# Optimization experiments

Measured on AMD Instinct MI355X. Metric: run time of the kernel, lower is better.

The kernel has to match this reference:

```python
import jax, jax.numpy as jnp
import numpy as np

N = 50000
E = 1600000
D_IN = 256
D_OUT = 256
NUM_SAMPLES = 5
LN_EPS = 1e-5


def setup_inputs() -> dict:
    key = jax.random.key(0)
    ks = jax.random.split(key, 6)
    x = jax.random.normal(ks[0], (N, D_IN), dtype=jnp.float32)
    adj_indices = jax.random.randint(ks[1], (2, E), 0, N, dtype=jnp.int32)
    adj_values = jax.random.uniform(ks[2], (E,), dtype=jnp.float32)
    mask = jax.random.uniform(ks[3], (NUM_SAMPLES, D_OUT), dtype=jnp.float32)
    # Xavier-uniform init as in reset_parameters
    limit_w = float(np.sqrt(6.0 / (D_IN + D_OUT)))
    weight = jax.random.uniform(ks[4], (D_IN, D_OUT), dtype=jnp.float32,
                                minval=-limit_w, maxval=limit_w)
    limit_b = float(np.sqrt(6.0 / (1 + D_OUT)))
    bias = jax.random.uniform(ks[5], (1, D_OUT), dtype=jnp.float32,
                              minval=-limit_b, maxval=limit_b)
    ln_gamma = jnp.ones((D_OUT,), dtype=jnp.float32)
    ln_beta = jnp.zeros((D_OUT,), dtype=jnp.float32)
    return {"x": x, "adj_indices": adj_indices, "adj_values": adj_values,
            "mask": mask, "weight": weight, "bias": bias,
            "ln_gamma": ln_gamma, "ln_beta": ln_beta}


def reference(x, adj_indices, adj_values, mask, weight, bias, ln_gamma, ln_beta):
    # dense transform: [N, D_in] @ [D_in, D_out]
    h = x @ weight
    # sparse adjacency spmm (COO): out[r] += v_e * h[c] for each edge e=(r,c)
    rows, cols = adj_indices[0], adj_indices[1]
    h = jax.ops.segment_sum(adj_values[:, None] * h[cols], rows, num_segments=N)
    # bias + ELU
    h = jax.nn.elu(h + bias)
    # LayerNorm over feature dim
    mu = jnp.mean(h, axis=-1, keepdims=True)
    var = jnp.var(h, axis=-1, keepdims=True)
    h = (h - mu) * jax.lax.rsqrt(var + LN_EPS) * ln_gamma + ln_beta
    # expand to num_samples and apply per-sample mask: [N, S, D_out]
    out = h[:, None, :] * mask[None, :, :]
    return out
```

## Files before the change

kernel.cpp:

```cpp
#include <hip/hip_runtime.h>
#include <math.h>

#define NNODES 50000
#define D 256
#define NSAMP 5
#define LN_EPS 1e-5f
#define NB 196
#define BCAP 9216
#define ACHUNK 8192

typedef __bf16 bf16;
typedef __attribute__((ext_vector_type(8))) __bf16 bf16x8;
typedef __attribute__((ext_vector_type(4))) float f32x4;
typedef unsigned long long u64;

__device__ inline float bflo(unsigned int u) { return __uint_as_float(u << 16); }
__device__ inline float bfhi(unsigned int u) { return __uint_as_float(u & 0xffff0000u); }

__device__ inline u64 packrec(int r, int c, float v) {
    return (u64)(unsigned int)(c | (r << 16)) | ((u64)__float_as_uint(v) << 32);
}

__global__ void prep_kernel(const float* __restrict__ w, bf16* __restrict__ wt,
                            int* __restrict__ bcur) {
    const int b = blockIdx.x;
    if (b < D) {
        const int k = threadIdx.x;
        wt[(size_t)b * D + k] = (bf16)w[(size_t)k * D + b];
    } else {
        if (threadIdx.x < NB) bcur[threadIdx.x] = 0;
    }
}

__global__ __launch_bounds__(256) void gemm_binA_kernel(const float* __restrict__ x,
                                                        const bf16* __restrict__ wt,
                                                        bf16* __restrict__ h,
                                                        const int* __restrict__ rows,
                                                        const int* __restrict__ cols,
                                                        const float* __restrict__ vals,
                                                        int* __restrict__ bcur,
                                                        u64* __restrict__ binned,
                                                        int AB, int E) {
    if ((int)blockIdx.x < AB) {
        __shared__ int hist[NB];
        __shared__ int base[NB];
        for (int i = threadIdx.x; i < NB; i += 256) hist[i] = 0;
        __syncthreads();
        const int e0 = blockIdx.x * ACHUNK;
        const int e1 = min(e0 + ACHUNK, E);
        for (int e = e0 + threadIdx.x; e < e1; e += 256)
            atomicAdd(&hist[rows[e] >> 8], 1);
        __syncthreads();
        for (int i = threadIdx.x; i < NB; i += 256) {
            const int c = hist[i];
            base[i] = c ? atomicAdd(&bcur[i], c) : 0;
            hist[i] = 0;
        }
        __syncthreads();
        for (int e = e0 + threadIdx.x; e < e1; e += 256) {
            const int r = rows[e];
            const int b = r >> 8;
            const int k = base[b] + atomicAdd(&hist[b], 1);
            if (k < BCAP)
                binned[(size_t)b * BCAP + k] = packrec(r, cols[e], vals[e]);
        }
        return;
    }

    const int gb = blockIdx.x - AB;
    const int wave = threadIdx.x >> 6;
    const int lane = threadIdx.x & 63;
    const int row0 = gb * 64 + wave * 16;
    const int am = lane & 15;
    const int ag = lane >> 4;

    int arow = row0 + am;
    if (arow >= NNODES) arow = NNODES - 1;

    f32x4 acc[16];
#pragma unroll
    for (int n = 0; n < 16; ++n) acc[n] = (f32x4){0.f, 0.f, 0.f, 0.f};

#pragma unroll
    for (int kk = 0; kk < 8; ++kk) {
        const int kb = kk * 32 + ag * 8;
        const float* xp = x + (size_t)arow * D + kb;
        const f32x4 a0 = __builtin_nontemporal_load((const f32x4*)xp);
        const f32x4 a1 = __builtin_nontemporal_load((const f32x4*)(xp + 4));
        bf16x8 a;
        a[0] = (bf16)a0[0]; a[1] = (bf16)a0[1]; a[2] = (bf16)a0[2]; a[3] = (bf16)a0[3];
        a[4] = (bf16)a1[0]; a[5] = (bf16)a1[1]; a[6] = (bf16)a1[2]; a[7] = (bf16)a1[3];
#pragma unroll
        for (int n = 0; n < 16; ++n) {
            const bf16x8 b = *(const bf16x8*)(wt + (size_t)(n * 16 + am) * D + kb);
            acc[n] = __builtin_amdgcn_mfma_f32_16x16x32_bf16(a, b, acc[n], 0, 0, 0);
        }
    }

    const int drow = row0 + ag * 4;
#pragma unroll
    for (int r = 0; r < 4; ++r) {
        if (drow + r < NNODES) {
            bf16* hp = h + (size_t)(drow + r) * D + am;
#pragma unroll
            for (int n = 0; n < 16; ++n) hp[n * 16] = (bf16)acc[n][r];
        }
    }
}

__global__ __launch_bounds__(256) void sortB_kernel(const u64* __restrict__ binned,
                                                    const int* __restrict__ bcur,
                                                    u64* __restrict__ sorted,
                                                    int* __restrict__ rstart,
                                                    int* __restrict__ rcnt) {
    const int b = blockIdx.x;
    const int tid = threadIdx.x;
    const int cnt_b = min(bcur[b], BCAP);
    const u64* src = binned + (size_t)b * BCAP;

    __shared__ int hist[256];
    __shared__ int s[256];
    hist[tid] = 0;
    __syncthreads();
    for (int i = tid; i < cnt_b; i += 256)
        atomicAdd(&hist[(int)((src[i] >> 16) & 255)], 1);
    __syncthreads();
    const int v = hist[tid];
    s[tid] = v;
    __syncthreads();
    for (int d = 1; d < 256; d <<= 1) {
        const int t = (tid >= d) ? s[tid - d] : 0;
        __syncthreads();
        s[tid] += t;
        __syncthreads();
    }
    const int excl = s[tid] - v;
    const int r = b * 256 + tid;
    if (r < NNODES) {
        rstart[r] = b * BCAP + excl;
        rcnt[r]   = v;
    }
    hist[tid] = excl;
    __syncthreads();
    for (int i = tid; i < cnt_b; i += 256) {
        const u64 rec = src[i];
        const int k = atomicAdd(&hist[(int)((rec >> 16) & 255)], 1);
        sorted[(size_t)b * BCAP + k] = rec;
    }
}

__global__ __launch_bounds__(256) void row_kernel(const unsigned short* __restrict__ hb,
                                                  const int* __restrict__ rstart,
                                                  const int* __restrict__ rcnt,
                                                  const u64* __restrict__ ep,
                                                  const float* __restrict__ bias,
                                                  const float* __restrict__ gamma,
                                                  const float* __restrict__ beta,
                                                  const float* __restrict__ mask,
                                                  float* __restrict__ out, int n) {
    const int wave = threadIdx.x >> 6;
    const int lane = threadIdx.x & 63;
    const int r = blockIdx.x * 4 + wave;
    if (r >= n) return;

    const int s = rstart[r];
    const int e = s + rcnt[r];

    float a0 = 0.f, a1 = 0.f, a2 = 0.f, a3 = 0.f;
    int i = s;
    for (; i + 3 < e; i += 4) {
        const u64 e0 = ep[i], e1 = ep[i + 1], e2 = ep[i + 2], e3 = ep[i + 3];
        const int c0 = (int)(e0 & 0xFFFF), c1 = (int)(e1 & 0xFFFF);
        const int c2 = (int)(e2 & 0xFFFF), c3 = (int)(e3 & 0xFFFF);
        const uint2 q0 = *(const uint2*)(hb + (size_t)c0 * D + lane * 4);
        const uint2 q1 = *(const uint2*)(hb + (size_t)c1 * D + lane * 4);
        const uint2 q2 = *(const uint2*)(hb + (size_t)c2 * D + lane * 4);
        const uint2 q3 = *(const uint2*)(hb + (size_t)c3 * D + lane * 4);
        const float v0 = __uint_as_float((unsigned int)(e0 >> 32));
        const float v1 = __uint_as_float((unsigned int)(e1 >> 32));
        const float v2 = __uint_as_float((unsigned int)(e2 >> 32));
        const float v3 = __uint_as_float((unsigned int)(e3 >> 32));
        a0 += v0 * bflo(q0.x) + v1 * bflo(q1.x) + v2 * bflo(q2.x) + v3 * bflo(q3.x);
        a1 += v0 * bfhi(q0.x) + v1 * bfhi(q1.x) + v2 * bfhi(q2.x) + v3 * bfhi(q3.x);
        a2 += v0 * bflo(q0.y) + v1 * bflo(q1.y) + v2 * bflo(q2.y) + v3 * bflo(q3.y);
        a3 += v0 * bfhi(q0.y) + v1 * bfhi(q1.y) + v2 * bfhi(q2.y) + v3 * bfhi(q3.y);
    }
    for (; i < e; ++i) {
        const u64 e0 = ep[i];
        const int c0 = (int)(e0 & 0xFFFF);
        const uint2 q0 = *(const uint2*)(hb + (size_t)c0 * D + lane * 4);
        const float v0 = __uint_as_float((unsigned int)(e0 >> 32));
        a0 += v0 * bflo(q0.x);
        a1 += v0 * bfhi(q0.x);
        a2 += v0 * bflo(q0.y);
        a3 += v0 * bfhi(q0.y);
    }

    const f32x4 b4 = *(const f32x4*)(bias + lane * 4);
    float x0 = a0 + b4[0], x1 = a1 + b4[1], x2 = a2 + b4[2], x3 = a3 + b4[3];
    x0 = x0 > 0.f ? x0 : expm1f(x0);
    x1 = x1 > 0.f ? x1 : expm1f(x1);
    x2 = x2 > 0.f ? x2 : expm1f(x2);
    x3 = x3 > 0.f ? x3 : expm1f(x3);

    float s1 = x0 + x1 + x2 + x3;
    float s2 = x0 * x0 + x1 * x1 + x2 * x2 + x3 * x3;
#pragma unroll
    for (int d = 1; d < 64; d <<= 1) {
        s1 += __shfl_xor(s1, d);
        s2 += __shfl_xor(s2, d);
    }
    const float mu   = s1 * (1.f / 256.f);
    const float var  = s2 * (1.f / 256.f) - mu * mu;
    const float rsig = rsqrtf(var + LN_EPS);

    const f32x4 g4  = *(const f32x4*)(gamma + lane * 4);
    const f32x4 be4 = *(const f32x4*)(beta + lane * 4);
    const float y0 = (x0 - mu) * rsig * g4[0] + be4[0];
    const float y1 = (x1 - mu) * rsig * g4[1] + be4[1];
    const float y2 = (x2 - mu) * rsig * g4[2] + be4[2];
    const float y3 = (x3 - mu) * rsig * g4[3] + be4[3];

#pragma unroll
    for (int smp = 0; smp < NSAMP; ++smp) {
        const f32x4 m4 = *(const f32x4*)(mask + smp * D + lane * 4);
        f32x4 o;
        o[0] = y0 * m4[0];
        o[1] = y1 * m4[1];
        o[2] = y2 * m4[2];
        o[3] = y3 * m4[3];
        __builtin_nontemporal_store(o, (f32x4*)(out + ((size_t)r * NSAMP + smp) * D + lane * 4));
    }
}

extern "C" void kernel_launch(void* const* d_in, const int* in_sizes, int n_in,
                              void* d_out, int out_size, void* d_ws, size_t ws_size,
                              hipStream_t stream) {
    const float* x     = (const float*)d_in[0];
    const int*   adj   = (const int*)d_in[1];
    const float* vals  = (const float*)d_in[2];
    const float* mask  = (const float*)d_in[3];
    const float* w     = (const float*)d_in[4];
    const float* bias  = (const float*)d_in[5];
    const float* gamma = (const float*)d_in[6];
    const float* beta  = (const float*)d_in[7];
    float*       out   = (float*)d_out;

    const int N = NNODES;
    const int E = in_sizes[2];
    const int GB = (N + 63) / 64;
    const int AB = (E + ACHUNK - 1) / ACHUNK;

    char* ws = (char*)d_ws;
    unsigned short* hb     = (unsigned short*)ws;
    u64*            sorted = (u64*)(hb + (size_t)N * D);
    u64*            binned = sorted + (size_t)NB * BCAP;
    bf16*           wt     = (bf16*)(binned + (size_t)NB * BCAP);
    int*            bcur   = (int*)((char*)wt + (size_t)D * D * 2);
    int*            rstart = bcur + 256;
    int*            rcnt   = rstart + N;

    prep_kernel<<<D + 1, 256, 0, stream>>>(w, wt, bcur);
    gemm_binA_kernel<<<AB + GB, 256, 0, stream>>>(x, wt, (bf16*)hb,
                                                  adj, adj + E, vals, bcur, binned, AB, E);
    sortB_kernel<<<NB, 256, 0, stream>>>(binned, bcur, sorted, rstart, rcnt);
    row_kernel<<<(N + 3) / 4, 256, 0, stream>>>(hb, rstart, rcnt, sorted,
                                                bias, gamma, beta, mask, out, N);
}
```

Before: 254.2 us.

## Pack sorted edges into 32-bit records with bf16 values; tile weight transpose

The sort kernel now emits 4-byte edge records: a 16-bit local column index plus a bf16-rounded edge value, replacing 8-byte records. This halves the edge-stream traffic read by the row aggregation kernel and its write traffic in the sort. The weight transpose now goes through a shared-memory tile for coalesced access, and bin counters are cleared with a memset. Edge values lose precision through bf16 rounding, which could affect accuracy tolerance.

```diff
diff --git a/kernel.cpp b/kernel.cpp
--- a/kernel.cpp
+++ b/kernel.cpp
@@ -13,22 +13,33 @@
 typedef __attribute__((ext_vector_type(8))) __bf16 bf16x8;
 typedef __attribute__((ext_vector_type(4))) float f32x4;
 typedef unsigned long long u64;
-
-__device__ inline float bflo(unsigned int u) { return __uint_as_float(u << 16); }
-__device__ inline float bfhi(unsigned int u) { return __uint_as_float(u & 0xffff0000u); }
+typedef unsigned int u32;
+
+__device__ inline float bflo(u32 u) { return __uint_as_float(u << 16); }
+__device__ inline float bfhi(u32 u) { return __uint_as_float(u & 0xffff0000u); }
 
 __device__ inline u64 packrec(int r, int c, float v) {
-    return (u64)(unsigned int)(c | (r << 16)) | ((u64)__float_as_uint(v) << 32);
-}
-
-__global__ void prep_kernel(const float* __restrict__ w, bf16* __restrict__ wt,
-                            int* __restrict__ bcur) {
-    const int b = blockIdx.x;
-    if (b < D) {
-        const int k = threadIdx.x;
-        wt[(size_t)b * D + k] = (bf16)w[(size_t)k * D + b];
-    } else {
-        if (threadIdx.x < NB) bcur[threadIdx.x] = 0;
+    return (u64)(u32)(c | (r << 16)) | ((u64)__float_as_uint(v) << 32);
+}
+
+__global__ __launch_bounds__(256) void prep_t_kernel(const float* __restrict__ w,
+                                                     bf16* __restrict__ wt) {
+    __shared__ float t[64][65];
+    const int bi = blockIdx.x >> 2;
+    const int bj = blockIdx.x & 3;
+    const int tid = threadIdx.x;
+#pragma unroll
+    for (int it = 0; it < 16; ++it) {
+        const int krow = (tid >> 6) + it * 4;
+        const int ncol = tid & 63;
+        t[krow][ncol] = w[(size_t)(bi * 64 + krow) * D + (bj * 64 + ncol)];
+    }
+    __syncthreads();
+#pragma unroll
+    for (int it = 0; it < 16; ++it) {
+        const int nrow = (tid >> 6) + it * 4;
+        const int kcol = tid & 63;
+        wt[(size_t)(bj * 64 + nrow) * D + (bi * 64 + kcol)] = (bf16)t[kcol][nrow];
     }
 }
 
@@ -110,7 +121,7 @@
 
 __global__ __launch_bounds__(256) void sortB_kernel(const u64* __restrict__ binned,
                                                     const int* __restrict__ bcur,
-                                                    u64* __restrict__ sorted,
+                                                    u32* __restrict__ sorted,
                                                     int* __restrict__ rstart,
                                                     int* __restrict__ rcnt) {
     const int b = blockIdx.x;
@@ -119,22 +130,22 @@
     const u64* src = binned + (size_t)b * BCAP;
 
     __shared__ int hist[256];
-    __shared__ int s[256];
+    __shared__ int scn[256];
     hist[tid] = 0;
     __syncthreads();
     for (int i = tid; i < cnt_b; i += 256)
         atomicAdd(&hist[(int)((src[i] >> 16) & 255)], 1);
     __syncthreads();
     const int v = hist[tid];
-    s[tid] = v;
+    scn[tid] = v;
     __syncthreads();
     for (int d = 1; d < 256; d <<= 1) {
-        const int t = (tid >= d) ? s[tid - d] : 0;
-        __syncthreads();
-        s[tid] += t;
-        __syncthreads();
-    }
-    const int excl = s[tid] - v;
+        const int t = (tid >= d) ? scn[tid - d] : 0;
+        __syncthreads();
+        scn[tid] += t;
+        __syncthreads();
+    }
+    const int excl = scn[tid] - v;
     const int r = b * 256 + tid;
     if (r < NNODES) {
         rstart[r] = b * BCAP + excl;
@@ -145,14 +156,16 @@
     for (int i = tid; i < cnt_b; i += 256) {
         const u64 rec = src[i];
         const int k = atomicAdd(&hist[(int)((rec >> 16) & 255)], 1);
-        sorted[(size_t)b * BCAP + k] = rec;
+        const float vf = __uint_as_float((u32)(rec >> 32));
+        const u32 vb = __float_as_uint((float)(bf16)vf) & 0xffff0000u;
+        sorted[(size_t)b * BCAP + k] = (u32)(rec & 0xFFFF) | vb;
     }
 }
 
 __global__ __launch_bounds__(256) void row_kernel(const unsigned short* __restrict__ hb,
                                                   const int* __restrict__ rstart,
                                                   const int* __restrict__ rcnt,
-                                                  const u64* __restrict__ ep,
+                                                  const u32* __restrict__ ep,
                                                   const float* __restrict__ bias,
                                                   const float* __restrict__ gamma,
                                                   const float* __restrict__ beta,
@@ -169,27 +182,21 @@
     float a0 = 0.f, a1 = 0.f, a2 = 0.f, a3 = 0.f;
     int i = s;
     for (; i + 3 < e; i += 4) {
-        const u64 e0 = ep[i], e1 = ep[i + 1], e2 = ep[i + 2], e3 = ep[i + 3];
-        const int c0 = (int)(e0 & 0xFFFF), c1 = (int)(e1 & 0xFFFF);
-        const int c2 = (int)(e2 & 0xFFFF), c3 = (int)(e3 & 0xFFFF);
-        const uint2 q0 = *(const uint2*)(hb + (size_t)c0 * D + lane * 4);
-        const uint2 q1 = *(const uint2*)(hb + (size_t)c1 * D + lane * 4);
-        const uint2 q2 = *(const uint2*)(hb + (size_t)c2 * D + lane * 4);
-        const uint2 q3 = *(const uint2*)(hb + (size_t)c3 * D + lane * 4);
-        const float v0 = __uint_as_float((unsigned int)(e0 >> 32));
-        const float v1 = __uint_as_float((unsigned int)(e1 >> 32));
-        const float v2 = __uint_as_float((unsigned int)(e2 >> 32));
-        const float v3 = __uint_as_float((unsigned int)(e3 >> 32));
+        const u32 e0 = ep[i], e1 = ep[i + 1], e2 = ep[i + 2], e3 = ep[i + 3];
+        const uint2 q0 = *(const uint2*)(hb + (size_t)(e0 & 0xFFFF) * D + lane * 4);
+        const uint2 q1 = *(const uint2*)(hb + (size_t)(e1 & 0xFFFF) * D + lane * 4);
+        const uint2 q2 = *(const uint2*)(hb + (size_t)(e2 & 0xFFFF) * D + lane * 4);
+        const uint2 q3 = *(const uint2*)(hb + (size_t)(e3 & 0xFFFF) * D + lane * 4);
+        const float v0 = bfhi(e0), v1 = bfhi(e1), v2 = bfhi(e2), v3 = bfhi(e3);
         a0 += v0 * bflo(q0.x) + v1 * bflo(q1.x) + v2 * bflo(q2.x) + v3 * bflo(q3.x);
         a1 += v0 * bfhi(q0.x) + v1 * bfhi(q1.x) + v2 * bfhi(q2.x) + v3 * bfhi(q3.x);
         a2 += v0 * bflo(q0.y) + v1 * bflo(q1.y) + v2 * bflo(q2.y) + v3 * bflo(q3.y);
         a3 += v0 * bfhi(q0.y) + v1 * bfhi(q1.y) + v2 * bfhi(q2.y) + v3 * bfhi(q3.y);
     }
     for (; i < e; ++i) {
-        const u64 e0 = ep[i];
-        const int c0 = (int)(e0 & 0xFFFF);
-        const uint2 q0 = *(const uint2*)(hb + (size_t)c0 * D + lane * 4);
-        const float v0 = __uint_as_float((unsigned int)(e0 >> 32));
+        const u32 e0 = ep[i];
+        const uint2 q0 = *(const uint2*)(hb + (size_t)(e0 & 0xFFFF) * D + lane * 4);
+        const float v0 = bfhi(e0);
         a0 += v0 * bflo(q0.x);
         a1 += v0 * bfhi(q0.x);
         a2 += v0 * bflo(q0.y);
@@ -253,14 +260,15 @@
 
     char* ws = (char*)d_ws;
     unsigned short* hb     = (unsigned short*)ws;
-    u64*            sorted = (u64*)(hb + (size_t)N * D);
-    u64*            binned = sorted + (size_t)NB * BCAP;
+    u32*            sorted = (u32*)(hb + (size_t)N * D);
+    u64*            binned = (u64*)(sorted + (size_t)NB * BCAP);
     bf16*           wt     = (bf16*)(binned + (size_t)NB * BCAP);
     int*            bcur   = (int*)((char*)wt + (size_t)D * D * 2);
     int*            rstart = bcur + 256;
     int*            rcnt   = rstart + N;
 
-    prep_kernel<<<D + 1, 256, 0, stream>>>(w, wt, bcur);
+    hipMemsetAsync(bcur, 0, 256 * sizeof(int), stream);
+    prep_t_kernel<<<16, 256, 0, stream>>>(w, wt);
     gemm_binA_kernel<<<AB + GB, 256, 0, stream>>>(x, wt, (bf16*)hb,
                                                   adj, adj + E, vals, bcur, binned, AB, E);
     sortB_kernel<<<NB, 256, 0, stream>>>(binned, bcur, sorted, rstart, rcnt);
```

Result: no change. 252.1 us (-0.8%).
